# Performance work log

Measured on AMD Instinct MI355X. Metric: run time of the kernel, lower is better.

Reference implementation:

```python
import jax, jax.numpy as jnp
import numpy as np

IN, OUT, FP, B, S = 8192, 28672, 128, 32, 1


def setup_inputs() -> dict:
    key = jax.random.key(0)
    k = jax.random.split(key, 6)
    x = jax.random.normal(k[0], (B, S, IN), dtype=jnp.float32).astype(jnp.float16)
    # int8 quantized weight, stored as [OUT, IN]
    weight = jax.random.randint(k[1], (OUT, IN), -128, 128, dtype=jnp.int32).astype(jnp.int8)
    # per-output-column dequant scale (fp16, positive, small)
    scale_col = (jax.random.uniform(k[2], (1, OUT), dtype=jnp.float32) * 0.01 + 1e-4).astype(jnp.float16)
    # fp16 cache of the outlier weight columns [OUT, FP]
    weight_cache = (jax.random.normal(k[3], (OUT, FP), dtype=jnp.float32) * 0.02).astype(jnp.float16)
    bias = (jax.random.normal(k[4], (OUT,), dtype=jnp.float32) * 0.02).astype(jnp.float16)
    # sorted unique outlier column indices
    ind = jnp.sort(jax.random.permutation(k[5], IN)[:FP]).astype(jnp.int32)
    return {"x": x, "weight": weight, "scale_col": scale_col,
            "weight_cache": weight_cache, "bias": bias, "ind": ind}


def reference(x, weight, scale_col, weight_cache, bias, ind):
    out_features = weight.shape[0]
    shape = x.shape[:-1] + (out_features,)
    inputs = x.reshape(-1, x.shape[-1])                       # [M, IN] fp16
    # ExtractOutliersAndSetToZeros: gather outlier activation columns, zero them
    act_outliers = inputs[:, ind]                              # [M, FP] fp16
    tmp = inputs.at[:, ind].set(jnp.float16(0))                # [M, IN]
    # FindRowScale (bit=8): symmetric per-row int8 scale
    x_scale = jnp.max(jnp.abs(tmp), axis=1, keepdims=True) / jnp.float16(127)  # [M, 1]
    q_x = jnp.clip(jnp.round(tmp / x_scale), -128, 127).astype(jnp.int8)       # [M, IN]
    # int8FusedDequantize: int8 GEMM -> dequant with row/col scales -> add fp16 outlier GEMM
    y_int = jnp.matmul(q_x.astype(jnp.int32), weight.T.astype(jnp.int32))      # [M, OUT] int32
    y = y_int.astype(jnp.float16) * x_scale * scale_col                        # dequantize
    y = y + jnp.matmul(act_outliers, weight_cache.T)                           # outlier fp16 GEMM
    y = y + bias
    return y.reshape(shape)
```

## Files before the change

kernel.cpp:

```cpp
#include <hip/hip_runtime.h>
#include <hip/hip_fp16.h>

#define IN_F   8192
#define OUT_F  28672
#define NFP    128
#define NB     32
#define KQTOT  (IN_F / 4)

#define KC     4
#define KCHUNK (IN_F / KC)

#define WS_QPK  0
#define WS_XS   262144
#define WS_ACT  263168
#define WS_PART 524288

typedef int v4i  __attribute__((ext_vector_type(4)));
typedef int v16i __attribute__((ext_vector_type(16)));

__device__ __forceinline__ int pack8(int4 v) {
    return (v.x & 0xFF) | ((v.y & 0xFF) << 8) | ((v.z & 0xFF) << 16) | (v.w << 24);
}

__global__ __launch_bounds__(256) void quant_kernel(
    const float* __restrict__ x, const int* __restrict__ ind,
    int* __restrict__ q_pk, float* __restrict__ xs_out,
    float* __restrict__ act_out)
{
    __shared__ unsigned char flags[IN_F];
    __shared__ float redbuf[4];
    __shared__ float xs_sh;
    const int tid = threadIdx.x;
    const int b = blockIdx.x;

    int* fl4 = (int*)flags;
    for (int i = tid; i < IN_F / 4; i += 256) fl4[i] = 0;
    __syncthreads();
    if (tid < NFP) flags[ind[tid]] = 1;
    __syncthreads();

    const float* xrow = x + (size_t)b * IN_F;
    const float4* x4 = (const float4*)xrow;
    float mx = 0.f;
    for (int c = tid; c < IN_F / 4; c += 256) {
        float4 v = x4[c];
        int fw = fl4[c];
        if (!(fw & 0x000000FF)) mx = fmaxf(mx, fabsf(v.x));
        if (!(fw & 0x0000FF00)) mx = fmaxf(mx, fabsf(v.y));
        if (!(fw & 0x00FF0000)) mx = fmaxf(mx, fabsf(v.z));
        if (!(fw & 0xFF000000)) mx = fmaxf(mx, fabsf(v.w));
    }
    #pragma unroll
    for (int off = 32; off > 0; off >>= 1) {
        float o = __shfl_down(mx, off, 64);
        mx = o > mx ? o : mx;
    }
    if ((tid & 63) == 0) redbuf[tid >> 6] = mx;
    __syncthreads();
    if (tid == 0) {
        float m = redbuf[0];
        #pragma unroll
        for (int i = 1; i < 4; i++) m = redbuf[i] > m ? redbuf[i] : m;
        float xs = __half2float(__float2half_rn(m / 127.0f));
        xs_sh = xs;
        xs_out[b] = xs;
    }
    __syncthreads();
    const float xs = xs_sh;

    for (int c = tid; c < IN_F / 4; c += 256) {
        float4 v = x4[c];
        int fw = fl4[c];
        float ee[4];
        ee[0] = (fw & 0x000000FF) ? 0.f : v.x;
        ee[1] = (fw & 0x0000FF00) ? 0.f : v.y;
        ee[2] = (fw & 0x00FF0000) ? 0.f : v.z;
        ee[3] = (fw & 0xFF000000) ? 0.f : v.w;
        int pk = 0;
        #pragma unroll
        for (int j = 0; j < 4; j++) {
            float qf = __half2float(__float2half_rn(ee[j] / xs));
            float r = rintf(qf);
            r = fminf(fmaxf(r, -128.f), 127.f);
            int qi = (int)r;
            pk |= (qi & 0xFF) << (8 * j);
        }
        q_pk[(size_t)b * KQTOT + c] = pk;
    }
    if (tid < NFP) act_out[b * NFP + tid] = xrow[ind[tid]];
}

#define OT    64
#define KT    256
#define KQT   (KT / 4)
#define WROW  68
#define QROW  68
#define NTILE (KCHUNK / KT)

__device__ __forceinline__ void stage_tiles(
    const int* __restrict__ w, const int* __restrict__ q_pk,
    int* __restrict__ wp, int* __restrict__ qt,
    int tid, int blk_o, int k0)
{
    #pragma unroll 4
    for (int i = 0; i < 8; i++) {
        int u  = i * 128 + tid;
        int r  = u >> 4;
        int c4 = u & 15;
        const int* src = w + (size_t)(blk_o + r) * IN_F + k0 + c4 * 16;
        int4 a = *(const int4*)(src + 0);
        int4 b = *(const int4*)(src + 4);
        int4 c = *(const int4*)(src + 8);
        int4 d = *(const int4*)(src + 12);
        int4 pk = make_int4(pack8(a), pack8(b), pack8(c), pack8(d));
        *(int4*)&wp[r * WROW + c4 * 4] = pk;
    }
    #pragma unroll
    for (int i = 0; i < 4; i++) {
        int u  = i * 128 + tid;
        int bb = u >> 4;
        int c4 = u & 15;
        int4 v = *(const int4*)(q_pk + (size_t)bb * KQTOT + (k0 >> 2) + c4 * 4);
        *(int4*)&qt[bb * QROW + c4 * 4] = v;
    }
}

__global__ __launch_bounds__(128) void gemm_kernel(
    const int* __restrict__ w, const int* __restrict__ q_pk,
    int* __restrict__ part)
{
    __shared__ int w_p[2][OT * WROW] __attribute__((aligned(16)));
    __shared__ int q_t[2][NB * QROW] __attribute__((aligned(16)));

    const int tid  = threadIdx.x;
    const int wave = tid >> 6;
    const int lane = tid & 63;
    const int nl   = lane & 31;
    const int half = lane >> 5;

    const int kc    = blockIdx.x & (KC - 1);
    const int blk_o = (blockIdx.x >> 2) * OT;
    const int kbase = kc * KCHUNK;
    const int n = blk_o + wave * 32 + nl;

    v16i acc;
    #pragma unroll
    for (int r = 0; r < 16; r++) acc[r] = 0;

    stage_tiles(w, q_pk, w_p[0], q_t[0], tid, blk_o, kbase);
    __syncthreads();

    for (int t = 0; t < NTILE; ++t) {
        const int cur = t & 1;
        if (t + 1 < NTILE)
            stage_tiles(w, q_pk, w_p[cur ^ 1], q_t[cur ^ 1],
                        tid, blk_o, kbase + (t + 1) * KT);

        const int* qrow = &q_t[cur][nl * QROW + half * 4];
        const int* wrow = &w_p[cur][(wave * 32 + nl) * WROW + half * 4];
        #pragma unroll
        for (int s = 0; s < KT / 32; s++) {
            v4i a = *(const v4i*)(qrow + s * 8);
            v4i b = *(const v4i*)(wrow + s * 8);
            acc = __builtin_amdgcn_mfma_i32_32x32x32_i8(a, b, acc, 0, 0, 0);
        }
        __syncthreads();
    }

    #pragma unroll
    for (int r = 0; r < 16; r++) {
        int b = (r & 3) + 8 * (r >> 2) + 4 * half;
        part[((size_t)kc * NB + b) * OUT_F + n] = acc[r];
    }
}

__global__ __launch_bounds__(256) void epilogue_kernel(
    const int* __restrict__ part, const float* __restrict__ xs_ws,
    const float* __restrict__ act_ws, const float* __restrict__ sc,
    const float* __restrict__ wc, const float* __restrict__ bias,
    float* __restrict__ out)
{
    __shared__ float act_l[NB * NFP];
    __shared__ float xs_l[NB];
    const int tid = threadIdx.x;
    const int blk_o = blockIdx.x * 64;

    for (int i = tid; i < NB * NFP; i += 256) act_l[i] = act_ws[i];
    if (tid < NB) xs_l[tid] = xs_ws[tid];
    __syncthreads();

    const int nl = tid & 63;
    const int n  = blk_o + nl;
    const int b0 = (tid >> 6) * 8;
    const float scn = sc[n];
    const float bin = bias[n];
    const float* wcn = wc + (size_t)n * NFP;

    float dots[8];
    #pragma unroll
    for (int j = 0; j < 8; j++) dots[j] = 0.f;
    for (int u = 0; u < NFP; u += 4) {
        float4 wv = *(const float4*)(wcn + u);
        #pragma unroll
        for (int j = 0; j < 8; j++) {
            float4 av = *(const float4*)(&act_l[(b0 + j) * NFP + u]);
            dots[j] += av.x * wv.x + av.y * wv.y + av.z * wv.z + av.w * wv.w;
        }
    }

    #pragma unroll
    for (int j = 0; j < 8; j++) {
        const int b = b0 + j;
        const size_t idx = (size_t)b * OUT_F + n;
        int s = part[idx];
        #pragma unroll
        for (int k = 1; k < KC; k++) s += part[((size_t)k * NB + b) * OUT_F + n];
        out[idx] = (float)s * xs_l[b] * scn + dots[j] + bin;
    }
}

extern "C" void kernel_launch(void* const* d_in, const int* in_sizes, int n_in,
                              void* d_out, int out_size, void* d_ws, size_t ws_size,
                              hipStream_t stream) {
    const float* x    = (const float*)d_in[0];
    const int*   wgt  = (const int*)d_in[1];
    const float* scol = (const float*)d_in[2];
    const float* wch  = (const float*)d_in[3];
    const float* bias = (const float*)d_in[4];
    const int*   ind  = (const int*)d_in[5];
    float* out = (float*)d_out;

    int*   q_pk = (int*)((char*)d_ws + WS_QPK);
    float* xs   = (float*)((char*)d_ws + WS_XS);
    float* act  = (float*)((char*)d_ws + WS_ACT);
    int*   part = (int*)((char*)d_ws + WS_PART);

    quant_kernel<<<NB, 256, 0, stream>>>(x, ind, q_pk, xs, act);
    gemm_kernel<<<(OUT_F / OT) * KC, 128, 0, stream>>>(wgt, q_pk, part);
    epilogue_kernel<<<OUT_F / 64, 256, 0, stream>>>(part, xs, act, scol, wch, bias, out);
}
```

Baseline: 1.212 ms.

## Drop LDS staging in int8 GEMM, load MFMA fragments directly from global

Rewrites the GEMM kernel so that each lane loads its weight and activation fragments straight from global memory into registers, packs them and issues the MFMA. This removes the shared-memory double buffer and the barriers. The split-K factor grows from 4 to 8 and blocks become 256 threads covering 128 output columns, which raises parallelism for this memory-bound skinny GEMM. In exchange there is no explicit prefetch, each lane's loads are strided by row, and the epilogue has to sum twice as many partials, increasing workspace traffic.

```diff
diff --git a/kernel.cpp b/kernel.cpp
--- a/kernel.cpp
+++ b/kernel.cpp
@@ -7,8 +7,9 @@
 #define NB     32
 #define KQTOT  (IN_F / 4)
 
-#define KC     4
+#define KC     8
 #define KCHUNK (IN_F / KC)
+#define NSTEP  (KCHUNK / 32)
 
 #define WS_QPK  0
 #define WS_XS   262144
@@ -90,81 +91,42 @@
     if (tid < NFP) act_out[b * NFP + tid] = xrow[ind[tid]];
 }
 
-#define OT    64
-#define KT    256
-#define KQT   (KT / 4)
-#define WROW  68
-#define QROW  68
-#define NTILE (KCHUNK / KT)
-
-__device__ __forceinline__ void stage_tiles(
-    const int* __restrict__ w, const int* __restrict__ q_pk,
-    int* __restrict__ wp, int* __restrict__ qt,
-    int tid, int blk_o, int k0)
-{
-    #pragma unroll 4
-    for (int i = 0; i < 8; i++) {
-        int u  = i * 128 + tid;
-        int r  = u >> 4;
-        int c4 = u & 15;
-        const int* src = w + (size_t)(blk_o + r) * IN_F + k0 + c4 * 16;
-        int4 a = *(const int4*)(src + 0);
-        int4 b = *(const int4*)(src + 4);
-        int4 c = *(const int4*)(src + 8);
-        int4 d = *(const int4*)(src + 12);
-        int4 pk = make_int4(pack8(a), pack8(b), pack8(c), pack8(d));
-        *(int4*)&wp[r * WROW + c4 * 4] = pk;
-    }
-    #pragma unroll
-    for (int i = 0; i < 4; i++) {
-        int u  = i * 128 + tid;
-        int bb = u >> 4;
-        int c4 = u & 15;
-        int4 v = *(const int4*)(q_pk + (size_t)bb * KQTOT + (k0 >> 2) + c4 * 4);
-        *(int4*)&qt[bb * QROW + c4 * 4] = v;
-    }
-}
-
-__global__ __launch_bounds__(128) void gemm_kernel(
+__global__ __launch_bounds__(256) void gemm_kernel(
     const int* __restrict__ w, const int* __restrict__ q_pk,
     int* __restrict__ part)
 {
-    __shared__ int w_p[2][OT * WROW] __attribute__((aligned(16)));
-    __shared__ int q_t[2][NB * QROW] __attribute__((aligned(16)));
-
     const int tid  = threadIdx.x;
-    const int wave = tid >> 6;
+    const int wv   = tid >> 6;
     const int lane = tid & 63;
     const int nl   = lane & 31;
     const int half = lane >> 5;
 
-    const int kc    = blockIdx.x & (KC - 1);
-    const int blk_o = (blockIdx.x >> 2) * OT;
+    const int kc = blockIdx.x & (KC - 1);
+    const int ng = blockIdx.x >> 3;
+    const int n  = ng * 128 + wv * 32 + nl;
     const int kbase = kc * KCHUNK;
-    const int n = blk_o + wave * 32 + nl;
+
+    const int* wrow  = w + (size_t)n * IN_F + kbase + 16 * half;
+    const int* qbase = q_pk + (size_t)nl * KQTOT + (kbase >> 2) + 4 * half;
 
     v16i acc;
     #pragma unroll
     for (int r = 0; r < 16; r++) acc[r] = 0;
 
-    stage_tiles(w, q_pk, w_p[0], q_t[0], tid, blk_o, kbase);
-    __syncthreads();
-
-    for (int t = 0; t < NTILE; ++t) {
-        const int cur = t & 1;
-        if (t + 1 < NTILE)
-            stage_tiles(w, q_pk, w_p[cur ^ 1], q_t[cur ^ 1],
-                        tid, blk_o, kbase + (t + 1) * KT);
-
-        const int* qrow = &q_t[cur][nl * QROW + half * 4];
-        const int* wrow = &w_p[cur][(wave * 32 + nl) * WROW + half * 4];
-        #pragma unroll
-        for (int s = 0; s < KT / 32; s++) {
-            v4i a = *(const v4i*)(qrow + s * 8);
-            v4i b = *(const v4i*)(wrow + s * 8);
-            acc = __builtin_amdgcn_mfma_i32_32x32x32_i8(a, b, acc, 0, 0, 0);
-        }
-        __syncthreads();
+    #pragma unroll 4
+    for (int s = 0; s < NSTEP; ++s) {
+        const int* ws_ = wrow + 32 * s;
+        int4 a0 = *(const int4*)(ws_ + 0);
+        int4 a1 = *(const int4*)(ws_ + 4);
+        int4 a2 = *(const int4*)(ws_ + 8);
+        int4 a3 = *(const int4*)(ws_ + 12);
+        v4i afrag = *(const v4i*)(qbase + 8 * s);
+        v4i bfrag;
+        bfrag[0] = pack8(a0);
+        bfrag[1] = pack8(a1);
+        bfrag[2] = pack8(a2);
+        bfrag[3] = pack8(a3);
+        acc = __builtin_amdgcn_mfma_i32_32x32x32_i8(afrag, bfrag, acc, 0, 0, 0);
     }
 
     #pragma unroll
@@ -236,6 +198,6 @@
     int*   part = (int*)((char*)d_ws + WS_PART);
 
     quant_kernel<<<NB, 256, 0, stream>>>(x, ind, q_pk, xs, act);
-    gemm_kernel<<<(OUT_F / OT) * KC, 128, 0, stream>>>(wgt, q_pk, part);
+    gemm_kernel<<<(OUT_F / 128) * KC, 256, 0, stream>>>(wgt, q_pk, part);
     epilogue_kernel<<<OUT_F / 64, 256, 0, stream>>>(part, xs, act, scol, wch, bias, out);
 }
```

After: 1.262 ms. +4.1%, slower.
